# Optimization experiments

Measured on AMD Instinct MI355X. Metric: run time of the kernel, lower is better.

## Reference

```python
import jax, jax.numpy as jnp
import numpy as np

B = 128
E, IN, H, OUT, ZD = 6, 1664, 512, 618, 32


def setup_inputs() -> dict:
    key = jax.random.key(0)
    ks = jax.random.split(key, 9)
    scale = 0.05
    return {
        "p_prev": jax.random.normal(ks[0], (B, IN), dtype=jnp.float32),
        "blending_coef": jax.random.uniform(ks[1], (B, E), dtype=jnp.float32),
        "z": jax.random.normal(ks[2], (B, ZD), dtype=jnp.float32),
        "w_l1": jax.random.normal(ks[3], (E, IN, H), dtype=jnp.float32) * scale,
        "b_l1": jax.random.normal(ks[4], (E, H), dtype=jnp.float32) * scale,
        "w_l2": jax.random.normal(ks[5], (E, H + ZD, H), dtype=jnp.float32) * scale,
        "b_l2": jax.random.normal(ks[6], (E, H + ZD, H)[0:0] + (E, H), dtype=jnp.float32) * scale,
        "w_l3": jax.random.normal(ks[7], (E, H + ZD, OUT), dtype=jnp.float32) * scale,
        "b_l3": jax.random.normal(ks[8], (E, OUT), dtype=jnp.float32) * scale,
    }


def _moe_layer(x, coef, w, b, use_act=True):
    # Per-sample blended weight matmul, fused as a single contraction:
    # y[b,o] = sum_i x[b,i] * (sum_e coef[b,e] * w[e,i,o]) + sum_e coef[b,e] * b[e,o]
    y = jnp.einsum("bi,eio,be->bo", x, w, coef) + jnp.einsum("be,eo->bo", coef, b)
    return jax.nn.elu(y) if use_act else y


def reference(p_prev, blending_coef, z, w_l1, b_l1, w_l2, b_l2, w_l3, b_l3):
    x = _moe_layer(p_prev, blending_coef, w_l1, b_l1)              # [B, H]
    x = _moe_layer(jnp.concatenate([x, z], axis=-1), blending_coef, w_l2, b_l2)  # [B, H]
    x = _moe_layer(jnp.concatenate([x, z], axis=-1), blending_coef, w_l3, b_l3, use_act=False)  # [B, OUT]
    return x
```

## Files before the change

kernel.cpp:

```cpp
#include <hip/hip_runtime.h>
#include <math.h>

#define B 128
#define E 6
#define IN_DIM 1664
#define H_DIM 512
#define OUT_DIM 618
#define ZD 32
#define K2 544
#define S1 13
#define S23 9

typedef __attribute__((ext_vector_type(8))) short short8;
typedef __attribute__((ext_vector_type(4))) float f32x4;
union U128 { uint4 u4; short8 s8; ushort us[8]; };

__device__ __forceinline__ ushort f2bf(float f) {
    uint u = __float_as_uint(f);
    u += 0x7fffu + ((u >> 16) & 1u);
    return (ushort)(u >> 16);
}
__device__ __forceinline__ uint pk2(float a, float b) {
    return (uint)f2bf(a) | ((uint)f2bf(b) << 16);
}
__device__ __forceinline__ float elu1(float x) { return x < 0.f ? expm1f(x) : x; }


__global__ __launch_bounds__(256) void init_bias(
    const float* __restrict__ coef,
    const float* __restrict__ b1, const float* __restrict__ b2,
    const float* __restrict__ b3,
    float* __restrict__ y1, float* __restrict__ y2, float* __restrict__ out)
{
    const int idx = blockIdx.x * 256 + threadIdx.x;
    if (idx >= B * (2 * H_DIM + OUT_DIM)) return;
    const int b = idx / (2 * H_DIM + OUT_DIM);
    const int o = idx - b * (2 * H_DIM + OUT_DIM);
    float ce[E];
    #pragma unroll
    for (int e = 0; e < E; ++e) ce[e] = coef[b * E + e];
    float v = 0.f;
    if (o < H_DIM) {
        #pragma unroll
        for (int e = 0; e < E; ++e) v = fmaf(ce[e], b1[e * H_DIM + o], v);
        y1[b * H_DIM + o] = v;
    } else if (o < 2 * H_DIM) {
        const int oo = o - H_DIM;
        #pragma unroll
        for (int e = 0; e < E; ++e) v = fmaf(ce[e], b2[e * H_DIM + oo], v);
        y2[b * H_DIM + oo] = v;
    } else {
        const int oo = o - 2 * H_DIM;
        #pragma unroll
        for (int e = 0; e < E; ++e) v = fmaf(ce[e], b3[e * OUT_DIM + oo], v);
        out[b * OUT_DIM + oo] = v;
    }
}

__global__ __launch_bounds__(256) void gemm1(
    const float* __restrict__ x,
    const float* __restrict__ coef,
    const float* __restrict__ w,
    float* __restrict__ y1)
{
    const int tid = threadIdx.x;
    const int l = tid & 63, wv = tid >> 6;
    const int n0 = blockIdx.x * 32, kb0 = blockIdx.y * 4;
    const int tn = tid & 31, tkq = tid >> 5;
    const int lp = ((tkq >> 1) << 4) | (tn & 15);
    const int fI = tn >> 4, j0 = (tkq & 1) << 2;
    const int colW = n0 + tn;
    const int row0 = 32 * wv + (l & 15), row1 = row0 + 16, kq = l >> 4;

    __shared__ ushort bs[2][2][64][8];

    float ce0[E], ce1[E];
    #pragma unroll
    for (int e = 0; e < E; ++e) {
        ce0[e] = coef[row0 * E + e];
        ce1[e] = coef[row1 * E + e];
    }

    auto ld_B = [&](int s, float* r) {
        const int e = s % E, kb = kb0 + s / E;
        const float* src = w + ((size_t)e * IN_DIM + kb * 32 + tkq * 4) * H_DIM + colW;
        #pragma unroll
        for (int j = 0; j < 4; ++j) r[j] = src[(size_t)j * H_DIM];
    };
    auto ld_X = [&](int kb, float4* xr) {
        const float* p0 = x + (size_t)row0 * IN_DIM + kb * 32 + kq * 8;
        const float* p1 = x + (size_t)row1 * IN_DIM + kb * 32 + kq * 8;
        xr[0] = *reinterpret_cast<const float4*>(p0);
        xr[1] = *reinterpret_cast<const float4*>(p0 + 4);
        xr[2] = *reinterpret_cast<const float4*>(p1);
        xr[3] = *reinterpret_cast<const float4*>(p1 + 4);
    };

    f32x4 acc00 = {0.f,0.f,0.f,0.f}, acc01 = {0.f,0.f,0.f,0.f};
    f32x4 acc10 = {0.f,0.f,0.f,0.f}, acc11 = {0.f,0.f,0.f,0.f};

    float wreg[2][4];
    float4 xreg[2][4];
    ld_B(0, wreg[0]); ld_B(1, wreg[1]);
    ld_X(kb0, xreg[0]); ld_X(kb0 + 1, xreg[1]);

    #pragma unroll
    for (int s = 0; s < E * 4; ++s) {
        const int pb_ = s & 1, e = s % E, kbi = s / E;
        uint2 pk;
        pk.x = pk2(wreg[pb_][0], wreg[pb_][1]);
        pk.y = pk2(wreg[pb_][2], wreg[pb_][3]);
        *reinterpret_cast<uint2*>(&bs[pb_][fI][lp][j0]) = pk;

        const float4* xc = xreg[kbi & 1];
        U128 a0, a1;
        a0.us[0] = f2bf(xc[0].x * ce0[e]); a0.us[1] = f2bf(xc[0].y * ce0[e]);
        a0.us[2] = f2bf(xc[0].z * ce0[e]); a0.us[3] = f2bf(xc[0].w * ce0[e]);
        a0.us[4] = f2bf(xc[1].x * ce0[e]); a0.us[5] = f2bf(xc[1].y * ce0[e]);
        a0.us[6] = f2bf(xc[1].z * ce0[e]); a0.us[7] = f2bf(xc[1].w * ce0[e]);
        a1.us[0] = f2bf(xc[2].x * ce1[e]); a1.us[1] = f2bf(xc[2].y * ce1[e]);
        a1.us[2] = f2bf(xc[2].z * ce1[e]); a1.us[3] = f2bf(xc[2].w * ce1[e]);
        a1.us[4] = f2bf(xc[3].x * ce1[e]); a1.us[5] = f2bf(xc[3].y * ce1[e]);
        a1.us[6] = f2bf(xc[3].z * ce1[e]); a1.us[7] = f2bf(xc[3].w * ce1[e]);

        if (s + 2 < E * 4) ld_B(s + 2, wreg[pb_]);
        if (e == E - 1 && kbi + 2 < 4)
            ld_X(kb0 + kbi + 2, xreg[kbi & 1]);

        __syncthreads();
        U128 b0, b1;
        b0.u4 = *reinterpret_cast<const uint4*>(&bs[pb_][0][l][0]);
        b1.u4 = *reinterpret_cast<const uint4*>(&bs[pb_][1][l][0]);
        acc00 = __builtin_amdgcn_mfma_f32_16x16x32_bf16(a0.s8, b0.s8, acc00, 0, 0, 0);
        acc01 = __builtin_amdgcn_mfma_f32_16x16x32_bf16(a0.s8, b1.s8, acc01, 0, 0, 0);
        acc10 = __builtin_amdgcn_mfma_f32_16x16x32_bf16(a1.s8, b0.s8, acc10, 0, 0, 0);
        acc11 = __builtin_amdgcn_mfma_f32_16x16x32_bf16(a1.s8, b1.s8, acc11, 0, 0, 0);
    }

    const int colB = n0 + (l & 15);
    const int rsub = (l >> 4) << 2;
    #pragma unroll
    for (int mi = 0; mi < 2; ++mi) {
        const int row = wv * 32 + mi * 16 + rsub;
        const f32x4 c0 = mi ? acc10 : acc00;
        const f32x4 c1 = mi ? acc11 : acc01;
        #pragma unroll
        for (int r = 0; r < 4; ++r) {
            atomicAdd(&y1[(size_t)(row + r) * H_DIM + colB],      c0[r]);
            atomicAdd(&y1[(size_t)(row + r) * H_DIM + colB + 16], c1[r]);
        }
    }
}

template<int KPB, bool ZS, int NW, bool GUARD>
__device__ __forceinline__ void gemm_mid_body(
    const float* __restrict__ yin,
    const float* __restrict__ coef,
    const float* __restrict__ z,
    const float* __restrict__ w,
    float* __restrict__ yout,
    int nt, int kb0, ushort (*bs)[2][64][8])
{
    constexpr int NS = E * KPB;
    const int tid = threadIdx.x;
    const int l = tid & 63, wv = tid >> 6;
    const int n0 = nt * 32;
    const int tn = tid & 31, tkq = tid >> 5;
    const int lp = ((tkq >> 1) << 4) | (tn & 15);
    const int fI = tn >> 4, j0 = (tkq & 1) << 2;
    const int colW = n0 + tn;
    const int row0 = 32 * wv + (l & 15), row1 = row0 + 16, kq = l >> 4;

    float ce0[E], ce1[E];
    #pragma unroll
    for (int e = 0; e < E; ++e) {
        ce0[e] = coef[row0 * E + e];
        ce1[e] = coef[row1 * E + e];
    }

    float v0[KPB * 8], v1[KPB * 8];
    if (ZS) {
        const float4 za = *reinterpret_cast<const float4*>(z + row0 * ZD + kq * 8);
        const float4 zb = *reinterpret_cast<const float4*>(z + row0 * ZD + kq * 8 + 4);
        const float4 zc = *reinterpret_cast<const float4*>(z + row1 * ZD + kq * 8);
        const float4 zd = *reinterpret_cast<const float4*>(z + row1 * ZD + kq * 8 + 4);
        v0[0]=za.x; v0[1]=za.y; v0[2]=za.z; v0[3]=za.w;
        v0[4]=zb.x; v0[5]=zb.y; v0[6]=zb.z; v0[7]=zb.w;
        v1[0]=zc.x; v1[1]=zc.y; v1[2]=zc.z; v1[3]=zc.w;
        v1[4]=zd.x; v1[5]=zd.y; v1[6]=zd.z; v1[7]=zd.w;
    } else {
        #pragma unroll
        for (int kbi = 0; kbi < KPB; ++kbi) {
            const int kk = (kb0 + kbi) * 32 + kq * 8;
            const float* p0 = yin + (size_t)row0 * H_DIM + kk;
            const float* p1 = yin + (size_t)row1 * H_DIM + kk;
            const float4 a = *reinterpret_cast<const float4*>(p0);
            const float4 b = *reinterpret_cast<const float4*>(p0 + 4);
            const float4 c = *reinterpret_cast<const float4*>(p1);
            const float4 d = *reinterpret_cast<const float4*>(p1 + 4);
            v0[kbi*8+0]=elu1(a.x); v0[kbi*8+1]=elu1(a.y);
            v0[kbi*8+2]=elu1(a.z); v0[kbi*8+3]=elu1(a.w);
            v0[kbi*8+4]=elu1(b.x); v0[kbi*8+5]=elu1(b.y);
            v0[kbi*8+6]=elu1(b.z); v0[kbi*8+7]=elu1(b.w);
            v1[kbi*8+0]=elu1(c.x); v1[kbi*8+1]=elu1(c.y);
            v1[kbi*8+2]=elu1(c.z); v1[kbi*8+3]=elu1(c.w);
            v1[kbi*8+4]=elu1(d.x); v1[kbi*8+5]=elu1(d.y);
            v1[kbi*8+6]=elu1(d.z); v1[kbi*8+7]=elu1(d.w);
        }
    }

    auto ld_B = [&](int s, float* r) {
        const int e = s % E, kb = kb0 + s / E;
        const float* src = w + ((size_t)e * K2 + kb * 32 + tkq * 4) * NW + colW;
        #pragma unroll
        for (int j = 0; j < 4; ++j)
            r[j] = (!GUARD || colW < NW) ? src[(size_t)j * NW] : 0.f;
    };

    f32x4 acc00 = {0.f,0.f,0.f,0.f}, acc01 = {0.f,0.f,0.f,0.f};
    f32x4 acc10 = {0.f,0.f,0.f,0.f}, acc11 = {0.f,0.f,0.f,0.f};

    float wreg[2][4];
    ld_B(0, wreg[0]);
    if (NS > 1) ld_B(1, wreg[1]);

    #pragma unroll
    for (int s = 0; s < NS; ++s) {
        const int pb_ = s & 1, e = s % E, kbi = s / E;
        uint2 pk;
        pk.x = pk2(wreg[pb_][0], wreg[pb_][1]);
        pk.y = pk2(wreg[pb_][2], wreg[pb_][3]);
        *reinterpret_cast<uint2*>(&bs[pb_][fI][lp][j0]) = pk;

        U128 a0, a1;
        #pragma unroll
        for (int j = 0; j < 8; ++j) {
            a0.us[j] = f2bf(v0[kbi * 8 + j] * ce0[e]);
            a1.us[j] = f2bf(v1[kbi * 8 + j] * ce1[e]);
        }

        if (s + 2 < NS) ld_B(s + 2, wreg[pb_]);

        __syncthreads();
        U128 b0, b1;
        b0.u4 = *reinterpret_cast<const uint4*>(&bs[pb_][0][l][0]);
        b1.u4 = *reinterpret_cast<const uint4*>(&bs[pb_][1][l][0]);
        acc00 = __builtin_amdgcn_mfma_f32_16x16x32_bf16(a0.s8, b0.s8, acc00, 0, 0, 0);
        acc01 = __builtin_amdgcn_mfma_f32_16x16x32_bf16(a0.s8, b1.s8, acc01, 0, 0, 0);
        acc10 = __builtin_amdgcn_mfma_f32_16x16x32_bf16(a1.s8, b0.s8, acc10, 0, 0, 0);
        acc11 = __builtin_amdgcn_mfma_f32_16x16x32_bf16(a1.s8, b1.s8, acc11, 0, 0, 0);
    }

    const int colB = n0 + (l & 15);
    const int rsub = (l >> 4) << 2;
    #pragma unroll
    for (int mi = 0; mi < 2; ++mi) {
        const int row = wv * 32 + mi * 16 + rsub;
        const f32x4 c0 = mi ? acc10 : acc00;
        const f32x4 c1 = mi ? acc11 : acc01;
        #pragma unroll
        for (int r = 0; r < 4; ++r) {
            if (!GUARD || colB < NW)
                atomicAdd(&yout[(size_t)(row + r) * NW + colB], c0[r]);
            if (!GUARD || colB + 16 < NW)
                atomicAdd(&yout[(size_t)(row + r) * NW + colB + 16], c1[r]);
        }
    }
}

__global__ __launch_bounds__(256) void gemm_l2(
    const float* __restrict__ y1, const float* __restrict__ coef,
    const float* __restrict__ z, const float* __restrict__ w2,
    float* __restrict__ y2)
{
    __shared__ ushort bs[2][2][64][8];
    const int nt = blockIdx.x, sp = blockIdx.y;
    if (sp < 8)
        gemm_mid_body<2, false, H_DIM, false>(y1, coef, z, w2, y2, nt, sp * 2, bs);
    else
        gemm_mid_body<1, true, H_DIM, false>(y1, coef, z, w2, y2, nt, 16, bs);
}

__global__ __launch_bounds__(256) void gemm_l3(
    const float* __restrict__ y2, const float* __restrict__ coef,
    const float* __restrict__ z, const float* __restrict__ w3,
    float* __restrict__ out)
{
    __shared__ ushort bs[2][2][64][8];
    const int nt = blockIdx.x, sp = blockIdx.y;
    if (sp < 8)
        gemm_mid_body<2, false, OUT_DIM, true>(y2, coef, z, w3, out, nt, sp * 2, bs);
    else
        gemm_mid_body<1, true, OUT_DIM, true>(y2, coef, z, w3, out, nt, 16, bs);
}

extern "C" void kernel_launch(void* const* d_in, const int* in_sizes, int n_in,
                              void* d_out, int out_size, void* d_ws, size_t ws_size,
                              hipStream_t stream)
{
    const float* p_prev = (const float*)d_in[0];
    const float* coef   = (const float*)d_in[1];
    const float* z      = (const float*)d_in[2];
    const float* w1     = (const float*)d_in[3];
    const float* b1     = (const float*)d_in[4];
    const float* w2     = (const float*)d_in[5];
    const float* b2     = (const float*)d_in[6];
    const float* w3     = (const float*)d_in[7];
    const float* b3     = (const float*)d_in[8];
    float* out = (float*)d_out;

    float* y1 = (float*)d_ws;
    float* y2 = y1 + (size_t)B * H_DIM;

    const int TOT = B * (2 * H_DIM + OUT_DIM);
    init_bias<<<(TOT + 255) / 256, 256, 0, stream>>>(coef, b1, b2, b3, y1, y2, out);
    gemm1<<<dim3(16, S1), 256, 0, stream>>>(p_prev, coef, w1, y1);
    gemm_l2<<<dim3(16, S23), 256, 0, stream>>>(y1, coef, z, w2, y2);
    gemm_l3<<<dim3(20, S23), 256, 0, stream>>>(y2, coef, z, w3, out);
}
```

Before: 49.05 us.

## Double split-K factor and route layer-3 output through workspace with last-block copy

Doubles the split-K grid for all three GEMMs so each block handles one or two K-chunks, which raises the block count to fill more CUs, and deepens the weight register prefetch to three stages. Layer 3 now accumulates atomically into a workspace buffer. A per-column-tile counter lets the last arriving block copy the finished tile into the output. This adds twice the atomic traffic and an extra copy pass plus a fence in exchange for more parallelism.

```diff
diff --git a/kernel.cpp b/kernel.cpp
--- a/kernel.cpp
+++ b/kernel.cpp
@@ -8,8 +8,8 @@
 #define OUT_DIM 618
 #define ZD 32
 #define K2 544
-#define S1 13
-#define S23 9
+#define S1 26
+#define S23 17
 
 typedef __attribute__((ext_vector_type(8))) short short8;
 typedef __attribute__((ext_vector_type(4))) float f32x4;
@@ -30,9 +30,11 @@
     const float* __restrict__ coef,
     const float* __restrict__ b1, const float* __restrict__ b2,
     const float* __restrict__ b3,
-    float* __restrict__ y1, float* __restrict__ y2, float* __restrict__ out)
+    float* __restrict__ y1, float* __restrict__ y2, float* __restrict__ y3,
+    int* __restrict__ cnt)
 {
     const int idx = blockIdx.x * 256 + threadIdx.x;
+    if (blockIdx.x == 0 && threadIdx.x < 32) cnt[threadIdx.x] = 0;
     if (idx >= B * (2 * H_DIM + OUT_DIM)) return;
     const int b = idx / (2 * H_DIM + OUT_DIM);
     const int o = idx - b * (2 * H_DIM + OUT_DIM);
@@ -53,7 +55,7 @@
         const int oo = o - 2 * H_DIM;
         #pragma unroll
         for (int e = 0; e < E; ++e) v = fmaf(ce[e], b3[e * OUT_DIM + oo], v);
-        out[b * OUT_DIM + oo] = v;
+        y3[b * OUT_DIM + oo] = v;
     }
 }
 
@@ -63,9 +65,10 @@
     const float* __restrict__ w,
     float* __restrict__ y1)
 {
+    constexpr int NS = E * 2;
     const int tid = threadIdx.x;
     const int l = tid & 63, wv = tid >> 6;
-    const int n0 = blockIdx.x * 32, kb0 = blockIdx.y * 4;
+    const int n0 = blockIdx.x * 32, kb0 = blockIdx.y * 2;
     const int tn = tid & 31, tkq = tid >> 5;
     const int lp = ((tkq >> 1) << 4) | (tn & 15);
     const int fI = tn >> 4, j0 = (tkq & 1) << 2;
@@ -87,32 +90,33 @@
         #pragma unroll
         for (int j = 0; j < 4; ++j) r[j] = src[(size_t)j * H_DIM];
     };
-    auto ld_X = [&](int kb, float4* xr) {
-        const float* p0 = x + (size_t)row0 * IN_DIM + kb * 32 + kq * 8;
-        const float* p1 = x + (size_t)row1 * IN_DIM + kb * 32 + kq * 8;
-        xr[0] = *reinterpret_cast<const float4*>(p0);
-        xr[1] = *reinterpret_cast<const float4*>(p0 + 4);
-        xr[2] = *reinterpret_cast<const float4*>(p1);
-        xr[3] = *reinterpret_cast<const float4*>(p1 + 4);
-    };
+
+    float4 xreg[2][4];
+    #pragma unroll
+    for (int kbi = 0; kbi < 2; ++kbi) {
+        const float* p0 = x + (size_t)row0 * IN_DIM + (kb0 + kbi) * 32 + kq * 8;
+        const float* p1 = x + (size_t)row1 * IN_DIM + (kb0 + kbi) * 32 + kq * 8;
+        xreg[kbi][0] = *reinterpret_cast<const float4*>(p0);
+        xreg[kbi][1] = *reinterpret_cast<const float4*>(p0 + 4);
+        xreg[kbi][2] = *reinterpret_cast<const float4*>(p1);
+        xreg[kbi][3] = *reinterpret_cast<const float4*>(p1 + 4);
+    }
 
     f32x4 acc00 = {0.f,0.f,0.f,0.f}, acc01 = {0.f,0.f,0.f,0.f};
     f32x4 acc10 = {0.f,0.f,0.f,0.f}, acc11 = {0.f,0.f,0.f,0.f};
 
-    float wreg[2][4];
-    float4 xreg[2][4];
-    ld_B(0, wreg[0]); ld_B(1, wreg[1]);
-    ld_X(kb0, xreg[0]); ld_X(kb0 + 1, xreg[1]);
-
-    #pragma unroll
-    for (int s = 0; s < E * 4; ++s) {
-        const int pb_ = s & 1, e = s % E, kbi = s / E;
+    float wreg[3][4];
+    ld_B(0, wreg[0]); ld_B(1, wreg[1]); ld_B(2, wreg[2]);
+
+    #pragma unroll
+    for (int s = 0; s < NS; ++s) {
+        const int rs = s % 3, pb_ = s & 1, e = s % E, kbi = s / E;
         uint2 pk;
-        pk.x = pk2(wreg[pb_][0], wreg[pb_][1]);
-        pk.y = pk2(wreg[pb_][2], wreg[pb_][3]);
+        pk.x = pk2(wreg[rs][0], wreg[rs][1]);
+        pk.y = pk2(wreg[rs][2], wreg[rs][3]);
         *reinterpret_cast<uint2*>(&bs[pb_][fI][lp][j0]) = pk;
 
-        const float4* xc = xreg[kbi & 1];
+        const float4* xc = xreg[kbi];
         U128 a0, a1;
         a0.us[0] = f2bf(xc[0].x * ce0[e]); a0.us[1] = f2bf(xc[0].y * ce0[e]);
         a0.us[2] = f2bf(xc[0].z * ce0[e]); a0.us[3] = f2bf(xc[0].w * ce0[e]);
@@ -123,9 +127,7 @@
         a1.us[4] = f2bf(xc[3].x * ce1[e]); a1.us[5] = f2bf(xc[3].y * ce1[e]);
         a1.us[6] = f2bf(xc[3].z * ce1[e]); a1.us[7] = f2bf(xc[3].w * ce1[e]);
 
-        if (s + 2 < E * 4) ld_B(s + 2, wreg[pb_]);
-        if (e == E - 1 && kbi + 2 < 4)
-            ld_X(kb0 + kbi + 2, xreg[kbi & 1]);
+        if (s + 3 < NS) ld_B(s + 3, wreg[rs]);
 
         __syncthreads();
         U128 b0, b1;
@@ -152,16 +154,18 @@
     }
 }
 
-template<int KPB, bool ZS, int NW, bool GUARD>
+template<bool ZS, int NW, bool GUARD, bool FIX>
 __device__ __forceinline__ void gemm_mid_body(
     const float* __restrict__ yin,
     const float* __restrict__ coef,
     const float* __restrict__ z,
     const float* __restrict__ w,
     float* __restrict__ yout,
+    float* __restrict__ out,
+    int* __restrict__ cnt,
     int nt, int kb0, ushort (*bs)[2][64][8])
 {
-    constexpr int NS = E * KPB;
+    constexpr int NS = E;
     const int tid = threadIdx.x;
     const int l = tid & 63, wv = tid >> 6;
     const int n0 = nt * 32;
@@ -178,7 +182,7 @@
         ce1[e] = coef[row1 * E + e];
     }
 
-    float v0[KPB * 8], v1[KPB * 8];
+    float v0[8], v1[8];
     if (ZS) {
         const float4 za = *reinterpret_cast<const float4*>(z + row0 * ZD + kq * 8);
         const float4 zb = *reinterpret_cast<const float4*>(z + row0 * ZD + kq * 8 + 4);
@@ -189,29 +193,21 @@
         v1[0]=zc.x; v1[1]=zc.y; v1[2]=zc.z; v1[3]=zc.w;
         v1[4]=zd.x; v1[5]=zd.y; v1[6]=zd.z; v1[7]=zd.w;
     } else {
-        #pragma unroll
-        for (int kbi = 0; kbi < KPB; ++kbi) {
-            const int kk = (kb0 + kbi) * 32 + kq * 8;
-            const float* p0 = yin + (size_t)row0 * H_DIM + kk;
-            const float* p1 = yin + (size_t)row1 * H_DIM + kk;
-            const float4 a = *reinterpret_cast<const float4*>(p0);
-            const float4 b = *reinterpret_cast<const float4*>(p0 + 4);
-            const float4 c = *reinterpret_cast<const float4*>(p1);
-            const float4 d = *reinterpret_cast<const float4*>(p1 + 4);
-            v0[kbi*8+0]=elu1(a.x); v0[kbi*8+1]=elu1(a.y);
-            v0[kbi*8+2]=elu1(a.z); v0[kbi*8+3]=elu1(a.w);
-            v0[kbi*8+4]=elu1(b.x); v0[kbi*8+5]=elu1(b.y);
-            v0[kbi*8+6]=elu1(b.z); v0[kbi*8+7]=elu1(b.w);
-            v1[kbi*8+0]=elu1(c.x); v1[kbi*8+1]=elu1(c.y);
-            v1[kbi*8+2]=elu1(c.z); v1[kbi*8+3]=elu1(c.w);
-            v1[kbi*8+4]=elu1(d.x); v1[kbi*8+5]=elu1(d.y);
-            v1[kbi*8+6]=elu1(d.z); v1[kbi*8+7]=elu1(d.w);
-        }
+        const int kk = kb0 * 32 + kq * 8;
+        const float* p0 = yin + (size_t)row0 * H_DIM + kk;
+        const float* p1 = yin + (size_t)row1 * H_DIM + kk;
+        const float4 a = *reinterpret_cast<const float4*>(p0);
+        const float4 b = *reinterpret_cast<const float4*>(p0 + 4);
+        const float4 c = *reinterpret_cast<const float4*>(p1);
+        const float4 d = *reinterpret_cast<const float4*>(p1 + 4);
+        v0[0]=elu1(a.x); v0[1]=elu1(a.y); v0[2]=elu1(a.z); v0[3]=elu1(a.w);
+        v0[4]=elu1(b.x); v0[5]=elu1(b.y); v0[6]=elu1(b.z); v0[7]=elu1(b.w);
+        v1[0]=elu1(c.x); v1[1]=elu1(c.y); v1[2]=elu1(c.z); v1[3]=elu1(c.w);
+        v1[4]=elu1(d.x); v1[5]=elu1(d.y); v1[6]=elu1(d.z); v1[7]=elu1(d.w);
     }
 
     auto ld_B = [&](int s, float* r) {
-        const int e = s % E, kb = kb0 + s / E;
-        const float* src = w + ((size_t)e * K2 + kb * 32 + tkq * 4) * NW + colW;
+        const float* src = w + ((size_t)s * K2 + kb0 * 32 + tkq * 4) * NW + colW;
         #pragma unroll
         for (int j = 0; j < 4; ++j)
             r[j] = (!GUARD || colW < NW) ? src[(size_t)j * NW] : 0.f;
@@ -220,26 +216,25 @@
     f32x4 acc00 = {0.f,0.f,0.f,0.f}, acc01 = {0.f,0.f,0.f,0.f};
     f32x4 acc10 = {0.f,0.f,0.f,0.f}, acc11 = {0.f,0.f,0.f,0.f};
 
-    float wreg[2][4];
-    ld_B(0, wreg[0]);
-    if (NS > 1) ld_B(1, wreg[1]);
+    float wreg[3][4];
+    ld_B(0, wreg[0]); ld_B(1, wreg[1]); ld_B(2, wreg[2]);
 
     #pragma unroll
     for (int s = 0; s < NS; ++s) {
-        const int pb_ = s & 1, e = s % E, kbi = s / E;
+        const int rs = s % 3, pb_ = s & 1;
         uint2 pk;
-        pk.x = pk2(wreg[pb_][0], wreg[pb_][1]);
-        pk.y = pk2(wreg[pb_][2], wreg[pb_][3]);
+        pk.x = pk2(wreg[rs][0], wreg[rs][1]);
+        pk.y = pk2(wreg[rs][2], wreg[rs][3]);
         *reinterpret_cast<uint2*>(&bs[pb_][fI][lp][j0]) = pk;
 
         U128 a0, a1;
         #pragma unroll
         for (int j = 0; j < 8; ++j) {
-            a0.us[j] = f2bf(v0[kbi * 8 + j] * ce0[e]);
-            a1.us[j] = f2bf(v1[kbi * 8 + j] * ce1[e]);
-        }
-
-        if (s + 2 < NS) ld_B(s + 2, wreg[pb_]);
+            a0.us[j] = f2bf(v0[j] * ce0[s]);
+            a1.us[j] = f2bf(v1[j] * ce1[s]);
+        }
+
+        if (s + 3 < NS) ld_B(s + 3, wreg[rs]);
 
         __syncthreads();
         U128 b0, b1;
@@ -266,6 +261,24 @@
                 atomicAdd(&yout[(size_t)(row + r) * NW + colB + 16], c1[r]);
         }
     }
+
+    if (FIX) {
+        __shared__ int last;
+        __threadfence();
+        if (tid == 0) {
+            const int old = atomicAdd(&cnt[nt], 1);
+            last = (old == S23 - 1);
+        }
+        __syncthreads();
+        if (last) {
+            __threadfence();
+            for (int i = tid; i < 32 * B; i += 256) {
+                const int row = i >> 5, col = n0 + (i & 31);
+                if (!GUARD || col < NW)
+                    out[(size_t)row * NW + col] = yout[(size_t)row * NW + col];
+            }
+        }
+    }
 }
 
 __global__ __launch_bounds__(256) void gemm_l2(
@@ -275,23 +288,27 @@
 {
     __shared__ ushort bs[2][2][64][8];
     const int nt = blockIdx.x, sp = blockIdx.y;
-    if (sp < 8)
-        gemm_mid_body<2, false, H_DIM, false>(y1, coef, z, w2, y2, nt, sp * 2, bs);
+    if (sp < 16)
+        gemm_mid_body<false, H_DIM, false, false>(y1, coef, z, w2, y2,
+                                                  nullptr, nullptr, nt, sp, bs);
     else
-        gemm_mid_body<1, true, H_DIM, false>(y1, coef, z, w2, y2, nt, 16, bs);
+        gemm_mid_body<true, H_DIM, false, false>(y1, coef, z, w2, y2,
+                                                 nullptr, nullptr, nt, 16, bs);
 }
 
 __global__ __launch_bounds__(256) void gemm_l3(
     const float* __restrict__ y2, const float* __restrict__ coef,
     const float* __restrict__ z, const float* __restrict__ w3,
-    float* __restrict__ out)
+    float* __restrict__ y3, float* __restrict__ out, int* __restrict__ cnt)
 {
     __shared__ ushort bs[2][2][64][8];
     const int nt = blockIdx.x, sp = blockIdx.y;
-    if (sp < 8)
-        gemm_mid_body<2, false, OUT_DIM, true>(y2, coef, z, w3, out, nt, sp * 2, bs);
+    if (sp < 16)
+        gemm_mid_body<false, OUT_DIM, true, true>(y2, coef, z, w3, y3,
+                                                  out, cnt, nt, sp, bs);
     else
-        gemm_mid_body<1, true, OUT_DIM, true>(y2, coef, z, w3, out, nt, 16, bs);
+        gemm_mid_body<true, OUT_DIM, true, true>(y2, coef, z, w3, y3,
+                                                 out, cnt, nt, 16, bs);
 }
 
 extern "C" void kernel_launch(void* const* d_in, const int* in_sizes, int n_in,
@@ -311,10 +328,13 @@
 
     float* y1 = (float*)d_ws;
     float* y2 = y1 + (size_t)B * H_DIM;
+    float* y3 = y2 + (size_t)B * H_DIM;
+    int* cnt  = (int*)(y3 + (size_t)B * OUT_DIM);
 
     const int TOT = B * (2 * H_DIM + OUT_DIM);
-    init_bias<<<(TOT + 255) / 256, 256, 0, stream>>>(coef, b1, b2, b3, y1, y2, out);
+    init_bias<<<(TOT + 255) / 256, 256, 0, stream>>>(coef, b1, b2, b3,
+                                                     y1, y2, y3, cnt);
     gemm1<<<dim3(16, S1), 256, 0, stream>>>(p_prev, coef, w1, y1);
     gemm_l2<<<dim3(16, S23), 256, 0, stream>>>(y1, coef, z, w2, y2);
-    gemm_l3<<<dim3(20, S23), 256, 0, stream>>>(y2, coef, z, w3, out);
-}
+    gemm_l3<<<dim3(20, S23), 256, 0, stream>>>(y2, coef, z, w3, y3, out, cnt);
+}
```

After: 68.89 us. +40.4%, slower.

## Load weight MFMA fragments directly into registers, dropping LDS staging and barriers

Applied to the files above, without the earlier changes.

Each lane now loads its B-operand fragment for the bf16 MFMA straight from global memory and converts it in registers. This removes the shared-memory transpose buffer and the per-step __syncthreads in all three GEMM kernels. In exchange, every one of the four waves in a block loads the same 32-column weight tile redundantly, so global and L2 traffic per block rises fourfold. It also doubles the per-lane conversion work and the registers held for prefetching.

```diff
diff --git a/kernel.cpp b/kernel.cpp
--- a/kernel.cpp
+++ b/kernel.cpp
@@ -20,9 +20,6 @@
     u += 0x7fffu + ((u >> 16) & 1u);
     return (ushort)(u >> 16);
 }
-__device__ __forceinline__ uint pk2(float a, float b) {
-    return (uint)f2bf(a) | ((uint)f2bf(b) << 16);
-}
 __device__ __forceinline__ float elu1(float x) { return x < 0.f ? expm1f(x) : x; }
 
 
@@ -63,16 +60,12 @@
     const float* __restrict__ w,
     float* __restrict__ y1)
 {
+    constexpr int NS = E * 4;
     const int tid = threadIdx.x;
     const int l = tid & 63, wv = tid >> 6;
     const int n0 = blockIdx.x * 32, kb0 = blockIdx.y * 4;
-    const int tn = tid & 31, tkq = tid >> 5;
-    const int lp = ((tkq >> 1) << 4) | (tn & 15);
-    const int fI = tn >> 4, j0 = (tkq & 1) << 2;
-    const int colW = n0 + tn;
     const int row0 = 32 * wv + (l & 15), row1 = row0 + 16, kq = l >> 4;
-
-    __shared__ ushort bs[2][2][64][8];
+    const int colf = n0 + (l & 15);
 
     float ce0[E], ce1[E];
     #pragma unroll
@@ -81,11 +74,14 @@
         ce1[e] = coef[row1 * E + e];
     }
 
-    auto ld_B = [&](int s, float* r) {
+    auto ld_Bfrag = [&](int s, float (*r)[8]) {
         const int e = s % E, kb = kb0 + s / E;
-        const float* src = w + ((size_t)e * IN_DIM + kb * 32 + tkq * 4) * H_DIM + colW;
-        #pragma unroll
-        for (int j = 0; j < 4; ++j) r[j] = src[(size_t)j * H_DIM];
+        const float* base = w + ((size_t)e * IN_DIM + kb * 32 + kq * 8) * H_DIM + colf;
+        #pragma unroll
+        for (int j = 0; j < 8; ++j) {
+            r[0][j] = base[(size_t)j * H_DIM];
+            r[1][j] = base[(size_t)j * H_DIM + 16];
+        }
     };
     auto ld_X = [&](int kb, float4* xr) {
         const float* p0 = x + (size_t)row0 * IN_DIM + kb * 32 + kq * 8;
@@ -99,18 +95,21 @@
     f32x4 acc00 = {0.f,0.f,0.f,0.f}, acc01 = {0.f,0.f,0.f,0.f};
     f32x4 acc10 = {0.f,0.f,0.f,0.f}, acc11 = {0.f,0.f,0.f,0.f};
 
-    float wreg[2][4];
+    float br[2][2][8];
     float4 xreg[2][4];
-    ld_B(0, wreg[0]); ld_B(1, wreg[1]);
+    ld_Bfrag(0, br[0]); ld_Bfrag(1, br[1]);
     ld_X(kb0, xreg[0]); ld_X(kb0 + 1, xreg[1]);
 
     #pragma unroll
-    for (int s = 0; s < E * 4; ++s) {
-        const int pb_ = s & 1, e = s % E, kbi = s / E;
-        uint2 pk;
-        pk.x = pk2(wreg[pb_][0], wreg[pb_][1]);
-        pk.y = pk2(wreg[pb_][2], wreg[pb_][3]);
-        *reinterpret_cast<uint2*>(&bs[pb_][fI][lp][j0]) = pk;
+    for (int s = 0; s < NS; ++s) {
+        const int rs = s & 1, e = s % E, kbi = s / E;
+
+        U128 b0, b1;
+        #pragma unroll
+        for (int j = 0; j < 8; ++j) {
+            b0.us[j] = f2bf(br[rs][0][j]);
+            b1.us[j] = f2bf(br[rs][1][j]);
+        }
 
         const float4* xc = xreg[kbi & 1];
         U128 a0, a1;
@@ -123,14 +122,10 @@
         a1.us[4] = f2bf(xc[3].x * ce1[e]); a1.us[5] = f2bf(xc[3].y * ce1[e]);
         a1.us[6] = f2bf(xc[3].z * ce1[e]); a1.us[7] = f2bf(xc[3].w * ce1[e]);
 
-        if (s + 2 < E * 4) ld_B(s + 2, wreg[pb_]);
+        if (s + 2 < NS) ld_Bfrag(s + 2, br[rs]);
         if (e == E - 1 && kbi + 2 < 4)
             ld_X(kb0 + kbi + 2, xreg[kbi & 1]);
 
-        __syncthreads();
-        U128 b0, b1;
-        b0.u4 = *reinterpret_cast<const uint4*>(&bs[pb_][0][l][0]);
-        b1.u4 = *reinterpret_cast<const uint4*>(&bs[pb_][1][l][0]);
         acc00 = __builtin_amdgcn_mfma_f32_16x16x32_bf16(a0.s8, b0.s8, acc00, 0, 0, 0);
         acc01 = __builtin_amdgcn_mfma_f32_16x16x32_bf16(a0.s8, b1.s8, acc01, 0, 0, 0);
         acc10 = __builtin_amdgcn_mfma_f32_16x16x32_bf16(a1.s8, b0.s8, acc10, 0, 0, 0);
@@ -159,17 +154,16 @@
     const float* __restrict__ z,
     const float* __restrict__ w,
     float* __restrict__ yout,
-    int nt, int kb0, ushort (*bs)[2][64][8])
+    int nt, int kb0)
 {
     constexpr int NS = E * KPB;
     const int tid = threadIdx.x;
     const int l = tid & 63, wv = tid >> 6;
     const int n0 = nt * 32;
-    const int tn = tid & 31, tkq = tid >> 5;
-    const int lp = ((tkq >> 1) << 4) | (tn & 15);
-    const int fI = tn >> 4, j0 = (tkq & 1) << 2;
-    const int colW = n0 + tn;
     const int row0 = 32 * wv + (l & 15), row1 = row0 + 16, kq = l >> 4;
+    const int colf = n0 + (l & 15);
+    const bool ok0 = !GUARD || colf < NW;
+    const bool ok1 = !GUARD || colf + 16 < NW;
 
     float ce0[E], ce1[E];
     #pragma unroll
@@ -209,28 +203,33 @@
         }
     }
 
-    auto ld_B = [&](int s, float* r) {
+    auto ld_Bfrag = [&](int s, float (*r)[8]) {
         const int e = s % E, kb = kb0 + s / E;
-        const float* src = w + ((size_t)e * K2 + kb * 32 + tkq * 4) * NW + colW;
-        #pragma unroll
-        for (int j = 0; j < 4; ++j)
-            r[j] = (!GUARD || colW < NW) ? src[(size_t)j * NW] : 0.f;
+        const float* base = w + ((size_t)e * K2 + kb * 32 + kq * 8) * NW + colf;
+        #pragma unroll
+        for (int j = 0; j < 8; ++j) {
+            r[0][j] = ok0 ? base[(size_t)j * NW] : 0.f;
+            r[1][j] = ok1 ? base[(size_t)j * NW + 16] : 0.f;
+        }
     };
 
     f32x4 acc00 = {0.f,0.f,0.f,0.f}, acc01 = {0.f,0.f,0.f,0.f};
     f32x4 acc10 = {0.f,0.f,0.f,0.f}, acc11 = {0.f,0.f,0.f,0.f};
 
-    float wreg[2][4];
-    ld_B(0, wreg[0]);
-    if (NS > 1) ld_B(1, wreg[1]);
+    float br[2][2][8];
+    ld_Bfrag(0, br[0]);
+    if (NS > 1) ld_Bfrag(1, br[1]);
 
     #pragma unroll
     for (int s = 0; s < NS; ++s) {
-        const int pb_ = s & 1, e = s % E, kbi = s / E;
-        uint2 pk;
-        pk.x = pk2(wreg[pb_][0], wreg[pb_][1]);
-        pk.y = pk2(wreg[pb_][2], wreg[pb_][3]);
-        *reinterpret_cast<uint2*>(&bs[pb_][fI][lp][j0]) = pk;
+        const int rs = s & 1, e = s % E, kbi = s / E;
+
+        U128 b0, b1;
+        #pragma unroll
+        for (int j = 0; j < 8; ++j) {
+            b0.us[j] = f2bf(br[rs][0][j]);
+            b1.us[j] = f2bf(br[rs][1][j]);
+        }
 
         U128 a0, a1;
         #pragma unroll
@@ -239,12 +238,8 @@
             a1.us[j] = f2bf(v1[kbi * 8 + j] * ce1[e]);
         }
 
-        if (s + 2 < NS) ld_B(s + 2, wreg[pb_]);
-
-        __syncthreads();
-        U128 b0, b1;
-        b0.u4 = *reinterpret_cast<const uint4*>(&bs[pb_][0][l][0]);
-        b1.u4 = *reinterpret_cast<const uint4*>(&bs[pb_][1][l][0]);
+        if (s + 2 < NS) ld_Bfrag(s + 2, br[rs]);
+
         acc00 = __builtin_amdgcn_mfma_f32_16x16x32_bf16(a0.s8, b0.s8, acc00, 0, 0, 0);
         acc01 = __builtin_amdgcn_mfma_f32_16x16x32_bf16(a0.s8, b1.s8, acc01, 0, 0, 0);
         acc10 = __builtin_amdgcn_mfma_f32_16x16x32_bf16(a1.s8, b0.s8, acc10, 0, 0, 0);
@@ -260,10 +255,8 @@
         const f32x4 c1 = mi ? acc11 : acc01;
         #pragma unroll
         for (int r = 0; r < 4; ++r) {
-            if (!GUARD || colB < NW)
-                atomicAdd(&yout[(size_t)(row + r) * NW + colB], c0[r]);
-            if (!GUARD || colB + 16 < NW)
-                atomicAdd(&yout[(size_t)(row + r) * NW + colB + 16], c1[r]);
+            if (ok0) atomicAdd(&yout[(size_t)(row + r) * NW + colB], c0[r]);
+            if (ok1) atomicAdd(&yout[(size_t)(row + r) * NW + colB + 16], c1[r]);
         }
     }
 }
@@ -273,12 +266,11 @@
     const float* __restrict__ z, const float* __restrict__ w2,
     float* __restrict__ y2)
 {
-    __shared__ ushort bs[2][2][64][8];
     const int nt = blockIdx.x, sp = blockIdx.y;
     if (sp < 8)
-        gemm_mid_body<2, false, H_DIM, false>(y1, coef, z, w2, y2, nt, sp * 2, bs);
+        gemm_mid_body<2, false, H_DIM, false>(y1, coef, z, w2, y2, nt, sp * 2);
     else
-        gemm_mid_body<1, true, H_DIM, false>(y1, coef, z, w2, y2, nt, 16, bs);
+        gemm_mid_body<1, true, H_DIM, false>(y1, coef, z, w2, y2, nt, 16);
 }
 
 __global__ __launch_bounds__(256) void gemm_l3(
@@ -286,12 +278,11 @@
     const float* __restrict__ z, const float* __restrict__ w3,
     float* __restrict__ out)
 {
-    __shared__ ushort bs[2][2][64][8];
     const int nt = blockIdx.x, sp = blockIdx.y;
     if (sp < 8)
-        gemm_mid_body<2, false, OUT_DIM, true>(y2, coef, z, w3, out, nt, sp * 2, bs);
+        gemm_mid_body<2, false, OUT_DIM, true>(y2, coef, z, w3, out, nt, sp * 2);
     else
-        gemm_mid_body<1, true, OUT_DIM, true>(y2, coef, z, w3, out, nt, 16, bs);
+        gemm_mid_body<1, true, OUT_DIM, true>(y2, coef, z, w3, out, nt, 16);
 }
 
 extern "C" void kernel_launch(void* const* d_in, const int* in_sizes, int n_in,
```

Measured after the change: 97.76 us. +99.3%, slower.

## Shrink GEMM tiles to 16 columns and finer K-splits for more blocks

Applied to the files above, without the earlier changes.

Each GEMM block now covers 16 output columns instead of 32 and fewer K blocks. gemm1 goes from 4 K-blocks to 2 per block, and the mid layers from 2 to 1. This roughly quadruples the grid size in every layer to fill more of the GPU's compute units on this small batch-128 problem. The cost is more atomicAdd traffic on the outputs, more redundant A-operand loads and bf16 conversions, and less MFMA work per barrier.

```diff
diff --git a/kernel.cpp b/kernel.cpp
--- a/kernel.cpp
+++ b/kernel.cpp
@@ -8,8 +8,8 @@
 #define OUT_DIM 618
 #define ZD 32
 #define K2 544
-#define S1 13
-#define S23 9
+#define S1 26
+#define S23 17
 
 typedef __attribute__((ext_vector_type(8))) short short8;
 typedef __attribute__((ext_vector_type(4))) float f32x4;
@@ -63,16 +63,16 @@
     const float* __restrict__ w,
     float* __restrict__ y1)
 {
+    constexpr int NS = E * 2;
     const int tid = threadIdx.x;
     const int l = tid & 63, wv = tid >> 6;
-    const int n0 = blockIdx.x * 32, kb0 = blockIdx.y * 4;
-    const int tn = tid & 31, tkq = tid >> 5;
-    const int lp = ((tkq >> 1) << 4) | (tn & 15);
-    const int fI = tn >> 4, j0 = (tkq & 1) << 2;
-    const int colW = n0 + tn;
+    const int n0 = blockIdx.x * 16, kb0 = blockIdx.y * 2;
+    const int tn = tid & 15, tq = tid >> 4;
+    const int lp = ((tq >> 2) << 4) | tn;
+    const int j0 = (2 * tq) & 7;
     const int row0 = 32 * wv + (l & 15), row1 = row0 + 16, kq = l >> 4;
 
-    __shared__ ushort bs[2][2][64][8];
+    __shared__ ushort bs[2][64][8];
 
     float ce0[E], ce1[E];
     #pragma unroll
@@ -83,9 +83,9 @@
 
     auto ld_B = [&](int s, float* r) {
         const int e = s % E, kb = kb0 + s / E;
-        const float* src = w + ((size_t)e * IN_DIM + kb * 32 + tkq * 4) * H_DIM + colW;
-        #pragma unroll
-        for (int j = 0; j < 4; ++j) r[j] = src[(size_t)j * H_DIM];
+        const float* src = w + ((size_t)e * IN_DIM + kb * 32 + 2 * tq) * H_DIM + n0 + tn;
+        r[0] = src[0];
+        r[1] = src[H_DIM];
     };
     auto ld_X = [&](int kb, float4* xr) {
         const float* p0 = x + (size_t)row0 * IN_DIM + kb * 32 + kq * 8;
@@ -96,23 +96,20 @@
         xr[3] = *reinterpret_cast<const float4*>(p1 + 4);
     };
 
-    f32x4 acc00 = {0.f,0.f,0.f,0.f}, acc01 = {0.f,0.f,0.f,0.f};
-    f32x4 acc10 = {0.f,0.f,0.f,0.f}, acc11 = {0.f,0.f,0.f,0.f};
-
-    float wreg[2][4];
+    f32x4 acc0 = {0.f,0.f,0.f,0.f}, acc1 = {0.f,0.f,0.f,0.f};
+
+    float wreg[2][2];
     float4 xreg[2][4];
     ld_B(0, wreg[0]); ld_B(1, wreg[1]);
     ld_X(kb0, xreg[0]); ld_X(kb0 + 1, xreg[1]);
 
     #pragma unroll
-    for (int s = 0; s < E * 4; ++s) {
-        const int pb_ = s & 1, e = s % E, kbi = s / E;
-        uint2 pk;
-        pk.x = pk2(wreg[pb_][0], wreg[pb_][1]);
-        pk.y = pk2(wreg[pb_][2], wreg[pb_][3]);
-        *reinterpret_cast<uint2*>(&bs[pb_][fI][lp][j0]) = pk;
-
-        const float4* xc = xreg[kbi & 1];
+    for (int s = 0; s < NS; ++s) {
+        const int rs = s & 1, pb_ = s & 1, e = s % E, kbi = s / E;
+
+        *reinterpret_cast<uint*>(&bs[pb_][lp][j0]) = pk2(wreg[rs][0], wreg[rs][1]);
+
+        const float4* xc = xreg[kbi];
         U128 a0, a1;
         a0.us[0] = f2bf(xc[0].x * ce0[e]); a0.us[1] = f2bf(xc[0].y * ce0[e]);
         a0.us[2] = f2bf(xc[0].z * ce0[e]); a0.us[3] = f2bf(xc[0].w * ce0[e]);
@@ -123,18 +120,13 @@
         a1.us[4] = f2bf(xc[3].x * ce1[e]); a1.us[5] = f2bf(xc[3].y * ce1[e]);
         a1.us[6] = f2bf(xc[3].z * ce1[e]); a1.us[7] = f2bf(xc[3].w * ce1[e]);
 
-        if (s + 2 < E * 4) ld_B(s + 2, wreg[pb_]);
-        if (e == E - 1 && kbi + 2 < 4)
-            ld_X(kb0 + kbi + 2, xreg[kbi & 1]);
+        if (s + 2 < NS) ld_B(s + 2, wreg[rs]);
 
         __syncthreads();
-        U128 b0, b1;
-        b0.u4 = *reinterpret_cast<const uint4*>(&bs[pb_][0][l][0]);
-        b1.u4 = *reinterpret_cast<const uint4*>(&bs[pb_][1][l][0]);
-        acc00 = __builtin_amdgcn_mfma_f32_16x16x32_bf16(a0.s8, b0.s8, acc00, 0, 0, 0);
-        acc01 = __builtin_amdgcn_mfma_f32_16x16x32_bf16(a0.s8, b1.s8, acc01, 0, 0, 0);
-        acc10 = __builtin_amdgcn_mfma_f32_16x16x32_bf16(a1.s8, b0.s8, acc10, 0, 0, 0);
-        acc11 = __builtin_amdgcn_mfma_f32_16x16x32_bf16(a1.s8, b1.s8, acc11, 0, 0, 0);
+        U128 b0;
+        b0.u4 = *reinterpret_cast<const uint4*>(&bs[pb_][l][0]);
+        acc0 = __builtin_amdgcn_mfma_f32_16x16x32_bf16(a0.s8, b0.s8, acc0, 0, 0, 0);
+        acc1 = __builtin_amdgcn_mfma_f32_16x16x32_bf16(a1.s8, b0.s8, acc1, 0, 0, 0);
     }
 
     const int colB = n0 + (l & 15);
@@ -142,34 +134,41 @@
     #pragma unroll
     for (int mi = 0; mi < 2; ++mi) {
         const int row = wv * 32 + mi * 16 + rsub;
-        const f32x4 c0 = mi ? acc10 : acc00;
-        const f32x4 c1 = mi ? acc11 : acc01;
-        #pragma unroll
-        for (int r = 0; r < 4; ++r) {
-            atomicAdd(&y1[(size_t)(row + r) * H_DIM + colB],      c0[r]);
-            atomicAdd(&y1[(size_t)(row + r) * H_DIM + colB + 16], c1[r]);
-        }
-    }
-}
-
-template<int KPB, bool ZS, int NW, bool GUARD>
+        const f32x4 c = mi ? acc1 : acc0;
+        #pragma unroll
+        for (int r = 0; r < 4; ++r)
+            atomicAdd(&y1[(size_t)(row + r) * H_DIM + colB], c[r]);
+    }
+}
+
+template<bool ZS, int NW, bool GUARD>
 __device__ __forceinline__ void gemm_mid_body(
     const float* __restrict__ yin,
     const float* __restrict__ coef,
     const float* __restrict__ z,
     const float* __restrict__ w,
     float* __restrict__ yout,
-    int nt, int kb0, ushort (*bs)[2][64][8])
-{
-    constexpr int NS = E * KPB;
+    int nt, int kb0, ushort (*bs)[64][8])
+{
+    constexpr int NS = E;
     const int tid = threadIdx.x;
     const int l = tid & 63, wv = tid >> 6;
-    const int n0 = nt * 32;
-    const int tn = tid & 31, tkq = tid >> 5;
-    const int lp = ((tkq >> 1) << 4) | (tn & 15);
-    const int fI = tn >> 4, j0 = (tkq & 1) << 2;
-    const int colW = n0 + tn;
+    const int n0 = nt * 16;
+    const int tn = tid & 15, tq = tid >> 4;
+    const int lp = ((tq >> 2) << 4) | tn;
+    const int j0 = (2 * tq) & 7;
     const int row0 = 32 * wv + (l & 15), row1 = row0 + 16, kq = l >> 4;
+    const bool okS = !GUARD || (n0 + tn) < NW;
+    const bool okC = !GUARD || (n0 + (l & 15)) < NW;
+
+    auto ld_B = [&](int s, float* r) {
+        const float* src = w + ((size_t)s * K2 + kb0 * 32 + 2 * tq) * NW + n0 + tn;
+        r[0] = okS ? src[0] : 0.f;
+        r[1] = okS ? src[NW] : 0.f;
+    };
+
+    float wreg[2][2];
+    ld_B(0, wreg[0]); ld_B(1, wreg[1]);
 
     float ce0[E], ce1[E];
     #pragma unroll
@@ -178,7 +177,7 @@
         ce1[e] = coef[row1 * E + e];
     }
 
-    float v0[KPB * 8], v1[KPB * 8];
+    float v0[8], v1[8];
     if (ZS) {
         const float4 za = *reinterpret_cast<const float4*>(z + row0 * ZD + kq * 8);
         const float4 zb = *reinterpret_cast<const float4*>(z + row0 * ZD + kq * 8 + 4);
@@ -189,66 +188,41 @@
         v1[0]=zc.x; v1[1]=zc.y; v1[2]=zc.z; v1[3]=zc.w;
         v1[4]=zd.x; v1[5]=zd.y; v1[6]=zd.z; v1[7]=zd.w;
     } else {
-        #pragma unroll
-        for (int kbi = 0; kbi < KPB; ++kbi) {
-            const int kk = (kb0 + kbi) * 32 + kq * 8;
-            const float* p0 = yin + (size_t)row0 * H_DIM + kk;
-            const float* p1 = yin + (size_t)row1 * H_DIM + kk;
-            const float4 a = *reinterpret_cast<const float4*>(p0);
-            const float4 b = *reinterpret_cast<const float4*>(p0 + 4);
-            const float4 c = *reinterpret_cast<const float4*>(p1);
-            const float4 d = *reinterpret_cast<const float4*>(p1 + 4);
-            v0[kbi*8+0]=elu1(a.x); v0[kbi*8+1]=elu1(a.y);
-            v0[kbi*8+2]=elu1(a.z); v0[kbi*8+3]=elu1(a.w);
-            v0[kbi*8+4]=elu1(b.x); v0[kbi*8+5]=elu1(b.y);
-            v0[kbi*8+6]=elu1(b.z); v0[kbi*8+7]=elu1(b.w);
-            v1[kbi*8+0]=elu1(c.x); v1[kbi*8+1]=elu1(c.y);
-            v1[kbi*8+2]=elu1(c.z); v1[kbi*8+3]=elu1(c.w);
-            v1[kbi*8+4]=elu1(d.x); v1[kbi*8+5]=elu1(d.y);
-            v1[kbi*8+6]=elu1(d.z); v1[kbi*8+7]=elu1(d.w);
+        const int kk = kb0 * 32 + kq * 8;
+        const float* p0 = yin + (size_t)row0 * H_DIM + kk;
+        const float* p1 = yin + (size_t)row1 * H_DIM + kk;
+        const float4 a = *reinterpret_cast<const float4*>(p0);
+        const float4 b = *reinterpret_cast<const float4*>(p0 + 4);
+        const float4 c = *reinterpret_cast<const float4*>(p1);
+        const float4 d = *reinterpret_cast<const float4*>(p1 + 4);
+        v0[0]=elu1(a.x); v0[1]=elu1(a.y); v0[2]=elu1(a.z); v0[3]=elu1(a.w);
+        v0[4]=elu1(b.x); v0[5]=elu1(b.y); v0[6]=elu1(b.z); v0[7]=elu1(b.w);
+        v1[0]=elu1(c.x); v1[1]=elu1(c.y); v1[2]=elu1(c.z); v1[3]=elu1(c.w);
+        v1[4]=elu1(d.x); v1[5]=elu1(d.y); v1[6]=elu1(d.z); v1[7]=elu1(d.w);
+    }
+
+    f32x4 acc0 = {0.f,0.f,0.f,0.f}, acc1 = {0.f,0.f,0.f,0.f};
+
+    #pragma unroll
+    for (int s = 0; s < NS; ++s) {
+        const int rs = s & 1, pb_ = s & 1;
+
+        *reinterpret_cast<uint*>(&bs[pb_][lp][j0]) = pk2(wreg[rs][0], wreg[rs][1]);
+
+        U128 a0, a1;
+        #pragma unroll
+        for (int j = 0; j < 8; ++j) {
+            a0.us[j] = f2bf(v0[j] * ce0[s]);
+            a1.us[j] = f2bf(v1[j] * ce1[s]);
         }
-    }
-
-    auto ld_B = [&](int s, float* r) {
-        const int e = s % E, kb = kb0 + s / E;
-        const float* src = w + ((size_t)e * K2 + kb * 32 + tkq * 4) * NW + colW;
-        #pragma unroll
-        for (int j = 0; j < 4; ++j)
-            r[j] = (!GUARD || colW < NW) ? src[(size_t)j * NW] : 0.f;
-    };
-
-    f32x4 acc00 = {0.f,0.f,0.f,0.f}, acc01 = {0.f,0.f,0.f,0.f};
-    f32x4 acc10 = {0.f,0.f,0.f,0.f}, acc11 = {0.f,0.f,0.f,0.f};
-
-    float wreg[2][4];
-    ld_B(0, wreg[0]);
-    if (NS > 1) ld_B(1, wreg[1]);
-
-    #pragma unroll
-    for (int s = 0; s < NS; ++s) {
-        const int pb_ = s & 1, e = s % E, kbi = s / E;
-        uint2 pk;
-        pk.x = pk2(wreg[pb_][0], wreg[pb_][1]);
-        pk.y = pk2(wreg[pb_][2], wreg[pb_][3]);
-        *reinterpret_cast<uint2*>(&bs[pb_][fI][lp][j0]) = pk;
-
-        U128 a0, a1;
-        #pragma unroll
-        for (int j = 0; j < 8; ++j) {
-            a0.us[j] = f2bf(v0[kbi * 8 + j] * ce0[e]);
-            a1.us[j] = f2bf(v1[kbi * 8 + j] * ce1[e]);
-        }
-
-        if (s + 2 < NS) ld_B(s + 2, wreg[pb_]);
+
+        if (s + 2 < NS) ld_B(s + 2, wreg[rs]);
 
         __syncthreads();
-        U128 b0, b1;
-        b0.u4 = *reinterpret_cast<const uint4*>(&bs[pb_][0][l][0]);
-        b1.u4 = *reinterpret_cast<const uint4*>(&bs[pb_][1][l][0]);
-        acc00 = __builtin_amdgcn_mfma_f32_16x16x32_bf16(a0.s8, b0.s8, acc00, 0, 0, 0);
-        acc01 = __builtin_amdgcn_mfma_f32_16x16x32_bf16(a0.s8, b1.s8, acc01, 0, 0, 0);
-        acc10 = __builtin_amdgcn_mfma_f32_16x16x32_bf16(a1.s8, b0.s8, acc10, 0, 0, 0);
-        acc11 = __builtin_amdgcn_mfma_f32_16x16x32_bf16(a1.s8, b1.s8, acc11, 0, 0, 0);
+        U128 b0;
+        b0.u4 = *reinterpret_cast<const uint4*>(&bs[pb_][l][0]);
+        acc0 = __builtin_amdgcn_mfma_f32_16x16x32_bf16(a0.s8, b0.s8, acc0, 0, 0, 0);
+        acc1 = __builtin_amdgcn_mfma_f32_16x16x32_bf16(a1.s8, b0.s8, acc1, 0, 0, 0);
     }
 
     const int colB = n0 + (l & 15);
@@ -256,15 +230,10 @@
     #pragma unroll
     for (int mi = 0; mi < 2; ++mi) {
         const int row = wv * 32 + mi * 16 + rsub;
-        const f32x4 c0 = mi ? acc10 : acc00;
-        const f32x4 c1 = mi ? acc11 : acc01;
-        #pragma unroll
-        for (int r = 0; r < 4; ++r) {
-            if (!GUARD || colB < NW)
-                atomicAdd(&yout[(size_t)(row + r) * NW + colB], c0[r]);
-            if (!GUARD || colB + 16 < NW)
-                atomicAdd(&yout[(size_t)(row + r) * NW + colB + 16], c1[r]);
-        }
+        const f32x4 c = mi ? acc1 : acc0;
+        #pragma unroll
+        for (int r = 0; r < 4; ++r)
+            if (okC) atomicAdd(&yout[(size_t)(row + r) * NW + colB], c[r]);
     }
 }
 
@@ -273,12 +242,12 @@
     const float* __restrict__ z, const float* __restrict__ w2,
     float* __restrict__ y2)
 {
-    __shared__ ushort bs[2][2][64][8];
+    __shared__ ushort bs[2][64][8];
     const int nt = blockIdx.x, sp = blockIdx.y;
-    if (sp < 8)
-        gemm_mid_body<2, false, H_DIM, false>(y1, coef, z, w2, y2, nt, sp * 2, bs);
+    if (sp < 16)
+        gemm_mid_body<false, H_DIM, false>(y1, coef, z, w2, y2, nt, sp, bs);
     else
-        gemm_mid_body<1, true, H_DIM, false>(y1, coef, z, w2, y2, nt, 16, bs);
+        gemm_mid_body<true, H_DIM, false>(y1, coef, z, w2, y2, nt, 16, bs);
 }
 
 __global__ __launch_bounds__(256) void gemm_l3(
@@ -286,12 +255,12 @@
     const float* __restrict__ z, const float* __restrict__ w3,
     float* __restrict__ out)
 {
-    __shared__ ushort bs[2][2][64][8];
+    __shared__ ushort bs[2][64][8];
     const int nt = blockIdx.x, sp = blockIdx.y;
-    if (sp < 8)
-        gemm_mid_body<2, false, OUT_DIM, true>(y2, coef, z, w3, out, nt, sp * 2, bs);
+    if (sp < 16)
+        gemm_mid_body<false, OUT_DIM, true>(y2, coef, z, w3, out, nt, sp, bs);
     else
-        gemm_mid_body<1, true, OUT_DIM, true>(y2, coef, z, w3, out, nt, 16, bs);
+        gemm_mid_body<true, OUT_DIM, true>(y2, coef, z, w3, out, nt, 16, bs);
 }
 
 extern "C" void kernel_launch(void* const* d_in, const int* in_sizes, int n_in,
@@ -314,7 +283,7 @@
 
     const int TOT = B * (2 * H_DIM + OUT_DIM);
     init_bias<<<(TOT + 255) / 256, 256, 0, stream>>>(coef, b1, b2, b3, y1, y2, out);
-    gemm1<<<dim3(16, S1), 256, 0, stream>>>(p_prev, coef, w1, y1);
-    gemm_l2<<<dim3(16, S23), 256, 0, stream>>>(y1, coef, z, w2, y2);
-    gemm_l3<<<dim3(20, S23), 256, 0, stream>>>(y2, coef, z, w3, out);
-}
+    gemm1<<<dim3(32, S1), 256, 0, stream>>>(p_prev, coef, w1, y1);
+    gemm_l2<<<dim3(32, S23), 256, 0, stream>>>(y1, coef, z, w2, y2);
+    gemm_l3<<<dim3(39, S23), 256, 0, stream>>>(y2, coef, z, w3, out);
+}
```

Measured after the change: 45.29 us. 1.08x faster.
